# Kernel optimization log

Measured on AMD Instinct MI355X. Metric: run time of the kernel, lower is better.

## Reference

```python
import jax, jax.numpy as jnp
import numpy as np

# ---- physics constraint targets (constants, precomputed with numpy) ----
_ARC = np.array([[-1,-1,-1],[2,2,2],[-1,-1,-1]], np.float32)
_CURV5 = np.array([[0,0,-1,0,0],[0,-1,2,-1,0],[-1,2,4,2,-1],[0,-1,2,-1,0],[0,0,-1,0,0]], np.float32)
_RAD = np.array([[0,-1,0],[-1,4,-1],[0,-1,0]], np.float32)
_TAN = np.array([[-1,0,-1],[0,4,0],[-1,0,-1]], np.float32)

def _bilinear_1d(a, out_n):
    # torch F.interpolate bilinear, align_corners=False, along axis 0
    n = a.shape[0]
    src = (np.arange(out_n) + 0.5) * n / out_n - 0.5
    i0 = np.clip(np.floor(src).astype(int), 0, n - 1)
    i1 = np.clip(i0 + 1, 0, n - 1)
    f = np.clip(src - np.floor(src), 0.0, 1.0).astype(np.float32)
    shp = (out_n,) + (1,) * (a.ndim - 1)
    return a[i0] * (1 - f).reshape(shp) + a[i1] * f.reshape(shp)

_CURV3 = _bilinear_1d(_bilinear_1d(_CURV5, 3).T, 3).T  # 5x5 -> 3x3 separable bilinear
CONSTRAINTS = jnp.asarray(np.stack([_ARC, _CURV3, _RAD, _TAN]))  # [4,3,3]

NUM_HEADS = 4
PHYSICS_WEIGHT = 0.1


def setup_inputs() -> dict:
    key = jax.random.key(0)
    ks = jax.random.split(key, 6)
    B, N, C = 8, 1024, 256
    return {
        "x": jax.random.normal(ks[0], (B, N, C), jnp.float32),
        "qkv_w": jax.random.normal(ks[1], (3 * C, C), jnp.float32) * (C ** -0.5),
        "qkv_b": jax.random.normal(ks[2], (3 * C,), jnp.float32) * 0.02,
        "proj_w": jax.random.normal(ks[3], (C, C), jnp.float32) * (C ** -0.5),
        "proj_b": jax.random.normal(ks[4], (C,), jnp.float32) * 0.02,
        "kernels": jax.random.normal(ks[5], (4, 3, 3), jnp.float32) * 0.1,
        "H": 32,
        "W": 32,
    }


def _physics_prior(x, kernels, H, W):
    # Original: depthwise conv each channel with each kernel, mean over kernels,
    # mean over channels, sigmoid, outer product. Conv + means are linear, so
    # mean-over-kernels and mean-over-channels commute with the (shared-kernel)
    # depthwise conv: conv(mean_C(x), mean_k(kernels)).
    B, N, C = x.shape
    xm = x.mean(axis=2).reshape(B, 1, H, W)            # [B,1,H,W]
    kmean = kernels.mean(axis=0)[None, None]           # [1,1,3,3] (OIHW)
    conv = jax.lax.conv_general_dilated(
        xm, kmean, window_strides=(1, 1), padding=((1, 1), (1, 1)),
        dimension_numbers=("NCHW", "OIHW", "NCHW"))
    amap = jax.nn.sigmoid(conv.reshape(B, N))          # [B,N]
    return amap[:, :, None] * amap[:, None, :]         # [B,N,N]


def _reg_loss(kernels):
    mse = jnp.mean((kernels - CONSTRAINTS) ** 2, axis=(1, 2)).sum()
    l1 = 0.01 * jnp.abs(kernels).sum()
    return mse + l1


def reference(x, qkv_w, qkv_b, proj_w, proj_b, kernels, H, W):
    B, N, C = x.shape
    hd = C // NUM_HEADS
    scale = hd ** -0.5
    qkv = (x @ qkv_w.T + qkv_b).reshape(B, N, 3, NUM_HEADS, hd)
    qkv = qkv.transpose(2, 0, 3, 1, 4)                 # [3,B,h,N,hd]
    q, k, v = qkv[0], qkv[1], qkv[2]
    attn = jnp.einsum("bhnd,bhmd->bhnm", q, k) * scale  # [B,h,N,N]
    prior = _physics_prior(x, kernels, H, W)            # [B,N,N]
    attn = attn + PHYSICS_WEIGHT * prior[:, None]
    attn = jax.nn.softmax(attn, axis=-1)                # dropout: eval mode (identity)
    out = jnp.einsum("bhnm,bhmd->bhnd", attn, v)
    out = out.transpose(0, 2, 1, 3).reshape(B, N, C)
    out = out @ proj_w.T + proj_b
    attention_weights = attn.mean(axis=1)               # [B,N,N]
    return out, attention_weights, _reg_loss(kernels)
```

## Files before the change

kernel.cpp:

```cpp
#include <hip/hip_runtime.h>
#include <cstdint>

typedef _Float16 h16;
typedef __attribute__((ext_vector_type(8))) _Float16 f16x8;
typedef __attribute__((ext_vector_type(4))) _Float16 f16x4;
typedef __attribute__((ext_vector_type(4))) float f32x4;

__global__ void k_xm(const float* __restrict__ x, float* __restrict__ xm) {
  int row = (blockIdx.x << 2) + (threadIdx.x >> 6);
  int lane = threadIdx.x & 63;
  const float* p = x + (size_t)row * 256;
  float s = p[lane] + p[lane + 64] + p[lane + 128] + p[lane + 192];
#pragma unroll
  for (int off = 32; off; off >>= 1) s += __shfl_xor(s, off);
  if (lane == 0) xm[row] = s * (1.0f / 256.0f);
}

__global__ void k_amap(const float* __restrict__ xm,
                       const float* __restrict__ kern,
                       float* __restrict__ amap) {
  int idx = blockIdx.x * 256 + threadIdx.x;
  int b = idx >> 10, n = idx & 1023;
  int y = n >> 5, xq = n & 31;
  float km[9];
#pragma unroll
  for (int i = 0; i < 9; ++i)
    km[i] = 0.25f * (kern[i] + kern[9 + i] + kern[18 + i] + kern[27 + i]);
  float acc = 0.f;
#pragma unroll
  for (int dy = 0; dy < 3; ++dy) {
#pragma unroll
    for (int dx = 0; dx < 3; ++dx) {
      int yy = y + dy - 1, xx = xq + dx - 1;
      if (yy >= 0 && yy < 32 && xx >= 0 && xx < 32)
        acc += km[dy * 3 + dx] * xm[(b << 10) + (yy << 5) + xx];
    }
  }
  amap[idx] = 1.0f / (1.0f + __expf(-acc));
}

__global__ void k_cast(const float* __restrict__ x, const float* __restrict__ qw,
                       const float* __restrict__ pw, h16* __restrict__ xh,
                       h16* __restrict__ qwh, h16* __restrict__ pwh) {
  int i4 = blockIdx.x * 256 + threadIdx.x;
  const float* src;
  h16* dst;
  int off;
  if (i4 < 524288) { src = x; dst = xh; off = i4; }
  else if (i4 < 573440) { src = qw; dst = qwh; off = i4 - 524288; }
  else { src = pw; dst = pwh; off = i4 - 573440; }
  float4 v = ((const float4*)src)[off];
  f16x4 o = {(h16)v.x, (h16)v.y, (h16)v.z, (h16)v.w};
  ((f16x4*)dst)[off] = o;
}

__global__ __launch_bounds__(128) void k_qkv(
    const h16* __restrict__ xh, const h16* __restrict__ qwh,
    const float* __restrict__ bias, h16* __restrict__ Qh,
    h16* __restrict__ Kh, h16* __restrict__ Vt) {
  const int w = threadIdx.x >> 6, lane = threadIdx.x & 63;
  const int g = lane >> 4, li = lane & 15;
  const int tile = blockIdx.x * 2 + w;
  const int tr = tile & 255, tc = tile >> 8;
  const int r0 = tr * 32, c0 = tc * 64;
  f32x4 acc[2][4];
#pragma unroll
  for (int mr = 0; mr < 2; ++mr)
#pragma unroll
    for (int nc = 0; nc < 4; ++nc) acc[mr][nc] = {0.f, 0.f, 0.f, 0.f};
  for (int ks = 0; ks < 8; ++ks) {
    int k0 = ks * 32 + g * 8;
    f16x8 a[2], bf[4];
#pragma unroll
    for (int mr = 0; mr < 2; ++mr)
      a[mr] = *(const f16x8*)(xh + (size_t)(r0 + mr * 16 + li) * 256 + k0);
#pragma unroll
    for (int nc = 0; nc < 4; ++nc)
      bf[nc] = *(const f16x8*)(qwh + (size_t)(c0 + nc * 16 + li) * 256 + k0);
#pragma unroll
    for (int mr = 0; mr < 2; ++mr)
#pragma unroll
      for (int nc = 0; nc < 4; ++nc)
        acc[mr][nc] = __builtin_amdgcn_mfma_f32_16x16x32_f16(a[mr], bf[nc],
                                                             acc[mr][nc], 0, 0, 0);
  }
  const int which = c0 >> 8;
  const int hh = (c0 >> 6) & 3;
#pragma unroll
  for (int nc = 0; nc < 4; ++nc) {
    int d = nc * 16 + li;
    float bv = bias[c0 + d];
#pragma unroll
    for (int mr = 0; mr < 2; ++mr) {
#pragma unroll
      for (int r = 0; r < 4; ++r) {
        int m = r0 + mr * 16 + g * 4 + r;
        int bq = m >> 10, n = m & 1023;
        float v = acc[mr][nc][r] + bv;
        size_t base = ((size_t)(bq * 4 + hh)) << 16;
        if (which == 0) Qh[base + (size_t)n * 64 + d] = (h16)v;
        else if (which == 1) Kh[base + (size_t)n * 64 + d] = (h16)v;
        else Vt[base + (size_t)d * 1024 + n] = (h16)v;
      }
    }
  }
}

__device__ __forceinline__ void compute_S(const h16* __restrict__ Kp,
                                          const float* __restrict__ am, int j0,
                                          const f16x8 (&qf)[2][2],
                                          const float (&am_r)[2][4], int g,
                                          int li, f32x4 (&s)[2][4]) {
  f16x8 kf[4][2];
#pragma unroll
  for (int nc = 0; nc < 4; ++nc)
#pragma unroll
    for (int ks = 0; ks < 2; ++ks)
      kf[nc][ks] =
          *(const f16x8*)(Kp + (size_t)(j0 + nc * 16 + li) * 64 + ks * 32 + g * 8);
#pragma unroll
  for (int mr = 0; mr < 2; ++mr)
#pragma unroll
    for (int nc = 0; nc < 4; ++nc) {
      f32x4 a = {0.f, 0.f, 0.f, 0.f};
      a = __builtin_amdgcn_mfma_f32_16x16x32_f16(qf[mr][0], kf[nc][0], a, 0, 0, 0);
      a = __builtin_amdgcn_mfma_f32_16x16x32_f16(qf[mr][1], kf[nc][1], a, 0, 0, 0);
      s[mr][nc] = a;
    }
#pragma unroll
  for (int mr = 0; mr < 2; ++mr)
#pragma unroll
    for (int nc = 0; nc < 4; ++nc) {
      float amc = am[j0 + nc * 16 + li];
#pragma unroll
      for (int r = 0; r < 4; ++r)
        s[mr][nc][r] = s[mr][nc][r] * 0.125f + am_r[mr][r] * amc;
    }
}

__global__ __launch_bounds__(256) void k_attn(
    const h16* __restrict__ Qh, const h16* __restrict__ Kh,
    const h16* __restrict__ Vt, const float* __restrict__ amap,
    h16* __restrict__ OHh, float* __restrict__ AW) {
  __shared__ __align__(16) unsigned char Pst[4][4096];
  const int tid = threadIdx.x;
  const int h = tid >> 6, lane = tid & 63, g = lane >> 4, li = lane & 15;
  const int b = blockIdx.x & 7, rt = blockIdx.x >> 3;
  const int r0 = rt * 32;
  const size_t base = ((size_t)(b * 4 + h)) << 16;
  const h16* Kp = Kh + base;
  const float* am = amap + (b << 10);

  f16x8 qf[2][2];
#pragma unroll
  for (int mr = 0; mr < 2; ++mr)
#pragma unroll
    for (int ks = 0; ks < 2; ++ks)
      qf[mr][ks] =
          *(const f16x8*)(Qh + base + (size_t)(r0 + mr * 16 + li) * 64 + ks * 32 + g * 8);

  float am_r[2][4];
#pragma unroll
  for (int mr = 0; mr < 2; ++mr)
#pragma unroll
    for (int r = 0; r < 4; ++r)
      am_r[mr][r] = 0.1f * am[r0 + mr * 16 + g * 4 + r];

  float m_run[2][4], l_run[2][4];
#pragma unroll
  for (int mr = 0; mr < 2; ++mr)
#pragma unroll
    for (int r = 0; r < 4; ++r) { m_run[mr][r] = -1e30f; l_run[mr][r] = 0.f; }

  for (int jt = 0; jt < 16; ++jt) {
    f32x4 s[2][4];
    compute_S(Kp, am, jt * 64, qf, am_r, g, li, s);
#pragma unroll
    for (int mr = 0; mr < 2; ++mr) {
#pragma unroll
      for (int r = 0; r < 4; ++r) {
        float mx = fmaxf(fmaxf(s[mr][0][r], s[mr][1][r]),
                         fmaxf(s[mr][2][r], s[mr][3][r]));
        mx = fmaxf(mx, __shfl_xor(mx, 1));
        mx = fmaxf(mx, __shfl_xor(mx, 2));
        mx = fmaxf(mx, __shfl_xor(mx, 4));
        mx = fmaxf(mx, __shfl_xor(mx, 8));
        float mnew = fmaxf(m_run[mr][r], mx);
        float ps = __expf(s[mr][0][r] - mnew) + __expf(s[mr][1][r] - mnew) +
                   __expf(s[mr][2][r] - mnew) + __expf(s[mr][3][r] - mnew);
        ps += __shfl_xor(ps, 1);
        ps += __shfl_xor(ps, 2);
        ps += __shfl_xor(ps, 4);
        ps += __shfl_xor(ps, 8);
        l_run[mr][r] = l_run[mr][r] * __expf(m_run[mr][r] - mnew) + ps;
        m_run[mr][r] = mnew;
      }
    }
  }
  float rinv[2][4];
#pragma unroll
  for (int mr = 0; mr < 2; ++mr)
#pragma unroll
    for (int r = 0; r < 4; ++r) rinv[mr][r] = 1.0f / l_run[mr][r];

  f32x4 o[2][4];
#pragma unroll
  for (int mr = 0; mr < 2; ++mr)
#pragma unroll
    for (int nd = 0; nd < 4; ++nd) o[mr][nd] = {0.f, 0.f, 0.f, 0.f};

  for (int jt = 0; jt < 16; ++jt) {
    const int j0 = jt * 64;
    f32x4 s[2][4];
    compute_S(Kp, am, j0, qf, am_r, g, li, s);
    __syncthreads();
#pragma unroll
    for (int mr = 0; mr < 2; ++mr) {
#pragma unroll
      for (int nc = 0; nc < 4; ++nc) {
        int colb = (nc * 16 + li) * 2;
#pragma unroll
        for (int r = 0; r < 4; ++r) {
          int row = mr * 16 + g * 4 + r;
          float p = __expf(s[mr][nc][r] - m_run[mr][r]) * rinv[mr][r];
          *(h16*)(&Pst[h][(row << 7) + (colb ^ ((row & 7) << 4))]) = (h16)p;
        }
      }
    }
    __syncthreads();
    f16x8 vf[4][2], af[2][2];
#pragma unroll
    for (int nd = 0; nd < 4; ++nd)
#pragma unroll
      for (int ks = 0; ks < 2; ++ks)
        vf[nd][ks] = *(const f16x8*)(Vt + base + (size_t)(nd * 16 + li) * 1024 +
                                     j0 + ks * 32 + g * 8);
#pragma unroll
    for (int mr = 0; mr < 2; ++mr)
#pragma unroll
      for (int ks = 0; ks < 2; ++ks) {
        int row = mr * 16 + li;
        int colb = (ks * 32 + g * 8) * 2;
        af[mr][ks] =
            *(const f16x8*)(&Pst[h][(row << 7) + (colb ^ ((row & 7) << 4))]);
      }
#pragma unroll
    for (int mr = 0; mr < 2; ++mr)
#pragma unroll
      for (int nd = 0; nd < 4; ++nd) {
        o[mr][nd] = __builtin_amdgcn_mfma_f32_16x16x32_f16(af[mr][0], vf[nd][0],
                                                           o[mr][nd], 0, 0, 0);
        o[mr][nd] = __builtin_amdgcn_mfma_f32_16x16x32_f16(af[mr][1], vf[nd][1],
                                                           o[mr][nd], 0, 0, 0);
      }
    {
      int row = tid >> 3, c8 = (tid & 7) * 8;
      float sum[8] = {0.f, 0.f, 0.f, 0.f, 0.f, 0.f, 0.f, 0.f};
#pragma unroll
      for (int hh = 0; hh < 4; ++hh) {
        f16x8 q = *(const f16x8*)(&Pst[hh][(row << 7) +
                                           ((c8 * 2) ^ ((row & 7) << 4))]);
#pragma unroll
        for (int i = 0; i < 8; ++i) sum[i] += (float)q[i];
      }
      float* dst = AW + ((size_t)b << 20) + (size_t)(r0 + row) * 1024 + j0 + c8;
      float4 o1 = {0.25f * sum[0], 0.25f * sum[1], 0.25f * sum[2], 0.25f * sum[3]};
      float4 o2 = {0.25f * sum[4], 0.25f * sum[5], 0.25f * sum[6], 0.25f * sum[7]};
      *(float4*)dst = o1;
      *(float4*)(dst + 4) = o2;
    }
  }
#pragma unroll
  for (int mr = 0; mr < 2; ++mr)
#pragma unroll
    for (int nd = 0; nd < 4; ++nd)
#pragma unroll
      for (int r = 0; r < 4; ++r)
        OHh[(size_t)((b << 10) + r0 + mr * 16 + g * 4 + r) * 256 + h * 64 +
            nd * 16 + li] = (h16)o[mr][nd][r];
}

__global__ __launch_bounds__(128) void k_proj(const h16* __restrict__ OHh,
                                              const h16* __restrict__ pwh,
                                              const float* __restrict__ bias,
                                              float* __restrict__ out) {
  const int w = threadIdx.x >> 6, lane = threadIdx.x & 63;
  const int g = lane >> 4, li = lane & 15;
  const int tile = blockIdx.x * 2 + w;
  const int tc = tile & 3, tr = tile >> 2;
  const int r0 = tr * 32, c0 = tc * 64;
  f32x4 acc[2][4];
#pragma unroll
  for (int mr = 0; mr < 2; ++mr)
#pragma unroll
    for (int nc = 0; nc < 4; ++nc) acc[mr][nc] = {0.f, 0.f, 0.f, 0.f};
  for (int ks = 0; ks < 8; ++ks) {
    int k0 = ks * 32 + g * 8;
    f16x8 a[2], bf[4];
#pragma unroll
    for (int mr = 0; mr < 2; ++mr)
      a[mr] = *(const f16x8*)(OHh + (size_t)(r0 + mr * 16 + li) * 256 + k0);
#pragma unroll
    for (int nc = 0; nc < 4; ++nc)
      bf[nc] = *(const f16x8*)(pwh + (size_t)(c0 + nc * 16 + li) * 256 + k0);
#pragma unroll
    for (int mr = 0; mr < 2; ++mr)
#pragma unroll
      for (int nc = 0; nc < 4; ++nc)
        acc[mr][nc] = __builtin_amdgcn_mfma_f32_16x16x32_f16(a[mr], bf[nc],
                                                             acc[mr][nc], 0, 0, 0);
  }
#pragma unroll
  for (int nc = 0; nc < 4; ++nc) {
    int c = c0 + nc * 16 + li;
    float bv = bias[c];
#pragma unroll
    for (int mr = 0; mr < 2; ++mr)
#pragma unroll
      for (int r = 0; r < 4; ++r) {
        int m = r0 + mr * 16 + g * 4 + r;
        out[(size_t)m * 256 + c] = acc[mr][nc][r] + bv;
      }
  }
}

__global__ void k_reg(const float* __restrict__ kern, float* __restrict__ out) {
  const float Cst[36] = {
      -1.f, -1.f, -1.f, 2.f, 2.f, 2.f, -1.f, -1.f, -1.f,
      -0.11111111f, 0.f, -0.11111111f, 0.f, 4.f, 0.f,
      -0.11111111f, 0.f, -0.11111111f,
      0.f, -1.f, 0.f, -1.f, 4.f, -1.f, 0.f, -1.f, 0.f,
      -1.f, 0.f, -1.f, 0.f, 4.f, 0.f, -1.f, 0.f, -1.f};
  int t = threadIdx.x;
  float v = 0.f;
  if (t < 36) {
    float kv = kern[t];
    float d = kv - Cst[t];
    v = d * d * (1.0f / 9.0f) + 0.01f * fabsf(kv);
  }
#pragma unroll
  for (int off = 32; off; off >>= 1) v += __shfl_xor(v, off);
  if (t == 0) out[0] = v;
}

extern "C" void kernel_launch(void* const* d_in, const int* in_sizes, int n_in,
                              void* d_out, int out_size, void* d_ws,
                              size_t ws_size, hipStream_t stream) {
  const float* x = (const float*)d_in[0];
  const float* qkv_w = (const float*)d_in[1];
  const float* qkv_b = (const float*)d_in[2];
  const float* proj_w = (const float*)d_in[3];
  const float* proj_b = (const float*)d_in[4];
  const float* kern = (const float*)d_in[5];

  float* out = (float*)d_out;
  float* aw = out + 2097152;
  float* rl = out + 10485760;

  float* xm = (float*)d_ws;
  float* amap = xm + 8192;
  h16* xh = (h16*)(amap + 8192);
  h16* qwh = xh + 2097152;
  h16* pwh = qwh + 196608;
  h16* Qh = pwh + 65536;
  h16* Kh = Qh + 2097152;
  h16* Vt = Kh + 2097152;
  h16* OHh = Vt + 2097152;

  k_xm<<<2048, 256, 0, stream>>>(x, xm);
  k_amap<<<32, 256, 0, stream>>>(xm, kern, amap);
  k_cast<<<2304, 256, 0, stream>>>(x, qkv_w, proj_w, xh, qwh, pwh);
  k_qkv<<<1536, 128, 0, stream>>>(xh, qwh, qkv_b, Qh, Kh, Vt);
  k_attn<<<256, 256, 0, stream>>>(Qh, Kh, Vt, amap, OHh, aw);
  k_proj<<<512, 128, 0, stream>>>(OHh, pwh, proj_b, out);
  k_reg<<<1, 64, 0, stream>>>(kern, rl);
}
```

Baseline: 215.2 us.

## Single-pass attention using Cauchy-Schwarz max bound and deferred normalization

Replaces the two-pass online-softmax attention with a single pass. A precomputed upper bound on each row's logits (query norm times the per-head max key norm, plus the prior term) serves as a fixed softmax shift, so no running max is needed. Unnormalized probabilities go to a global fp16 buffer, and a separate kernel applies the row normalization and averages over heads to write the attention weights. The key range is also split across two waves per head with an LDS reduction, and the x->fp16 cast is fused with the channel mean. The cost is extra global traffic for P and a risk that the loose bound underflows exp2 for rows whose logits sit far below it.

```diff
diff --git a/kernel.cpp b/kernel.cpp
--- a/kernel.cpp
+++ b/kernel.cpp
@@ -6,14 +6,35 @@
 typedef __attribute__((ext_vector_type(4))) _Float16 f16x4;
 typedef __attribute__((ext_vector_type(4))) float f32x4;
 
-__global__ void k_xm(const float* __restrict__ x, float* __restrict__ xm) {
-  int row = (blockIdx.x << 2) + (threadIdx.x >> 6);
-  int lane = threadIdx.x & 63;
-  const float* p = x + (size_t)row * 256;
-  float s = p[lane] + p[lane + 64] + p[lane + 128] + p[lane + 192];
-#pragma unroll
-  for (int off = 32; off; off >>= 1) s += __shfl_xor(s, off);
-  if (lane == 0) xm[row] = s * (1.0f / 256.0f);
+#define L2E 1.44269504f
+
+__global__ void k_cast(const float* __restrict__ x, const float* __restrict__ qw,
+                       const float* __restrict__ pw, h16* __restrict__ xh,
+                       h16* __restrict__ qwh, h16* __restrict__ pwh,
+                       float* __restrict__ xm) {
+  int bid = blockIdx.x, tid = threadIdx.x;
+  if (bid < 2048) {
+    int i4 = bid * 256 + tid;
+    float4 v = ((const float4*)x)[i4];
+    f16x4 o = {(h16)v.x, (h16)v.y, (h16)v.z, (h16)v.w};
+    ((f16x4*)xh)[i4] = o;
+    float s = v.x + v.y + v.z + v.w;
+#pragma unroll
+    for (int off = 32; off; off >>= 1) s += __shfl_xor(s, off);
+    if ((tid & 63) == 0) xm[i4 >> 6] = s * (1.0f / 256.0f);
+  } else {
+    int i4 = (bid - 2048) * 256 + tid;
+    if (i4 < 49152) {
+      float4 v = ((const float4*)qw)[i4];
+      f16x4 o = {(h16)v.x, (h16)v.y, (h16)v.z, (h16)v.w};
+      ((f16x4*)qwh)[i4] = o;
+    } else {
+      int j = i4 - 49152;
+      float4 v = ((const float4*)pw)[j];
+      f16x4 o = {(h16)v.x, (h16)v.y, (h16)v.z, (h16)v.w};
+      ((f16x4*)pwh)[j] = o;
+    }
+  }
 }
 
 __global__ void k_amap(const float* __restrict__ xm,
@@ -37,21 +58,6 @@
     }
   }
   amap[idx] = 1.0f / (1.0f + __expf(-acc));
-}
-
-__global__ void k_cast(const float* __restrict__ x, const float* __restrict__ qw,
-                       const float* __restrict__ pw, h16* __restrict__ xh,
-                       h16* __restrict__ qwh, h16* __restrict__ pwh) {
-  int i4 = blockIdx.x * 256 + threadIdx.x;
-  const float* src;
-  h16* dst;
-  int off;
-  if (i4 < 524288) { src = x; dst = xh; off = i4; }
-  else if (i4 < 573440) { src = qw; dst = qwh; off = i4 - 524288; }
-  else { src = pw; dst = pwh; off = i4 - 573440; }
-  float4 v = ((const float4*)src)[off];
-  f16x4 o = {(h16)v.x, (h16)v.y, (h16)v.z, (h16)v.w};
-  ((f16x4*)dst)[off] = o;
 }
 
 __global__ __launch_bounds__(128) void k_qkv(
@@ -106,178 +112,197 @@
   }
 }
 
-__device__ __forceinline__ void compute_S(const h16* __restrict__ Kp,
-                                          const float* __restrict__ am, int j0,
-                                          const f16x8 (&qf)[2][2],
-                                          const float (&am_r)[2][4], int g,
-                                          int li, f32x4 (&s)[2][4]) {
-  f16x8 kf[4][2];
-#pragma unroll
-  for (int nc = 0; nc < 4; ++nc)
-#pragma unroll
-    for (int ks = 0; ks < 2; ++ks)
-      kf[nc][ks] =
-          *(const f16x8*)(Kp + (size_t)(j0 + nc * 16 + li) * 64 + ks * 32 + g * 8);
-#pragma unroll
-  for (int mr = 0; mr < 2; ++mr)
+__global__ void k_knorm(const h16* __restrict__ Kh, float* __restrict__ Kmaxb) {
+  __shared__ float red[4];
+  const int tid = threadIdx.x;
+  const h16* base = Kh + ((size_t)blockIdx.x << 16);
+  float mx = 0.f;
+#pragma unroll
+  for (int i = 0; i < 4; ++i) {
+    int n = i * 256 + tid;
+    float s2 = 0.f;
+#pragma unroll
+    for (int ks = 0; ks < 8; ++ks) {
+      f16x8 v = *(const f16x8*)(base + (size_t)n * 64 + ks * 8);
+#pragma unroll
+      for (int e = 0; e < 8; ++e) {
+        float f = (float)v[e];
+        s2 += f * f;
+      }
+    }
+    mx = fmaxf(mx, s2);
+  }
+#pragma unroll
+  for (int off = 32; off; off >>= 1) mx = fmaxf(mx, __shfl_xor(mx, off));
+  if ((tid & 63) == 0) red[tid >> 6] = mx;
+  __syncthreads();
+  if (tid == 0) {
+    mx = fmaxf(fmaxf(red[0], red[1]), fmaxf(red[2], red[3]));
+    Kmaxb[blockIdx.x] = sqrtf(mx);
+  }
+}
+
+__global__ __launch_bounds__(512, 4) void k_attn(
+    const h16* __restrict__ Qh, const h16* __restrict__ Kh,
+    const h16* __restrict__ Vt, const float* __restrict__ amap,
+    const float* __restrict__ Kmaxb, h16* __restrict__ Pg,
+    float* __restrict__ rinvb, h16* __restrict__ OHh) {
+  __shared__ float am_s[1024];
+  __shared__ float Lsh[4][2][16];
+  __shared__ float Osh[4][16][64];
+  __shared__ __align__(16) unsigned char Pst[8][2048];
+
+  const int tid = threadIdx.x;
+  const int wave = tid >> 6, lane = tid & 63, g = lane >> 4, li = lane & 15;
+  const int h = wave >> 1, jh = wave & 1;
+  const int b = blockIdx.x & 7, rt = blockIdx.x >> 3;
+  const int r0 = rt * 16;
+  const int bh = b * 4 + h;
+  const size_t base = ((size_t)bh) << 16;
+
+  am_s[tid] = amap[(b << 10) + tid];
+  am_s[tid + 512] = amap[(b << 10) + 512 + tid];
+  __syncthreads();
+
+  f16x8 qf[2];
+#pragma unroll
+  for (int ks = 0; ks < 2; ++ks)
+    qf[ks] = *(const f16x8*)(Qh + base + (size_t)(r0 + li) * 64 + ks * 32 + g * 8);
+
+  float nq2 = 0.f;
+#pragma unroll
+  for (int ks = 0; ks < 2; ++ks)
+#pragma unroll
+    for (int e = 0; e < 8; ++e) {
+      float f = (float)qf[ks][e];
+      nq2 += f * f;
+    }
+  nq2 += __shfl_xor(nq2, 16);
+  nq2 += __shfl_xor(nq2, 32);
+  float c_li = 0.125f * sqrtf(nq2) * Kmaxb[bh] + 0.11f;
+  float cr2[4], amr2[4];
+#pragma unroll
+  for (int r = 0; r < 4; ++r) {
+    cr2[r] = __shfl(c_li, g * 4 + r) * L2E;
+    amr2[r] = 0.1f * L2E * am_s[r0 + g * 4 + r];
+  }
+
+  float lpart[4] = {0.f, 0.f, 0.f, 0.f};
+  f32x4 o[4];
+#pragma unroll
+  for (int nd = 0; nd < 4; ++nd) o[nd] = {0.f, 0.f, 0.f, 0.f};
+
+  for (int jj = 0; jj < 8; ++jj) {
+    const int j0 = (jh * 8 + jj) << 6;
+    f16x8 kf[4][2];
+#pragma unroll
+    for (int nc = 0; nc < 4; ++nc)
+#pragma unroll
+      for (int ks = 0; ks < 2; ++ks)
+        kf[nc][ks] = *(const f16x8*)(Kh + base + (size_t)(j0 + nc * 16 + li) * 64 +
+                                     ks * 32 + g * 8);
+    f32x4 s[4];
 #pragma unroll
     for (int nc = 0; nc < 4; ++nc) {
       f32x4 a = {0.f, 0.f, 0.f, 0.f};
-      a = __builtin_amdgcn_mfma_f32_16x16x32_f16(qf[mr][0], kf[nc][0], a, 0, 0, 0);
-      a = __builtin_amdgcn_mfma_f32_16x16x32_f16(qf[mr][1], kf[nc][1], a, 0, 0, 0);
-      s[mr][nc] = a;
-    }
-#pragma unroll
-  for (int mr = 0; mr < 2; ++mr)
+      a = __builtin_amdgcn_mfma_f32_16x16x32_f16(qf[0], kf[nc][0], a, 0, 0, 0);
+      a = __builtin_amdgcn_mfma_f32_16x16x32_f16(qf[1], kf[nc][1], a, 0, 0, 0);
+      s[nc] = a;
+    }
 #pragma unroll
     for (int nc = 0; nc < 4; ++nc) {
-      float amc = am[j0 + nc * 16 + li];
+      float amc = am_s[j0 + nc * 16 + li];
+      int colb = (nc * 16 + li) * 2;
+#pragma unroll
+      for (int r = 0; r < 4; ++r) {
+        float p = exp2f(s[nc][r] * (0.125f * L2E) + amr2[r] * amc - cr2[r]);
+        lpart[r] += p;
+        int row = g * 4 + r;
+        *(h16*)(&Pst[wave][(row << 7) + (colb ^ ((row & 7) << 4))]) = (h16)p;
+      }
+    }
+    f16x8 af[2];
+#pragma unroll
+    for (int ks = 0; ks < 2; ++ks) {
+      int cb = (ks * 32 + g * 8) * 2;
+      af[ks] = *(const f16x8*)(&Pst[wave][(li << 7) + (cb ^ ((li & 7) << 4))]);
+      *(f16x8*)(Pg + ((size_t)bh << 20) + (size_t)(r0 + li) * 1024 + j0 +
+                ks * 32 + g * 8) = af[ks];
+    }
+#pragma unroll
+    for (int nd = 0; nd < 4; ++nd) {
+      f16x8 v0 = *(const f16x8*)(Vt + base + (size_t)(nd * 16 + li) * 1024 + j0 +
+                                 g * 8);
+      f16x8 v1 = *(const f16x8*)(Vt + base + (size_t)(nd * 16 + li) * 1024 + j0 +
+                                 32 + g * 8);
+      o[nd] = __builtin_amdgcn_mfma_f32_16x16x32_f16(af[0], v0, o[nd], 0, 0, 0);
+      o[nd] = __builtin_amdgcn_mfma_f32_16x16x32_f16(af[1], v1, o[nd], 0, 0, 0);
+    }
+  }
+
+#pragma unroll
+  for (int r = 0; r < 4; ++r) {
+    lpart[r] += __shfl_xor(lpart[r], 1);
+    lpart[r] += __shfl_xor(lpart[r], 2);
+    lpart[r] += __shfl_xor(lpart[r], 4);
+    lpart[r] += __shfl_xor(lpart[r], 8);
+  }
+  if (li == 0) {
+#pragma unroll
+    for (int r = 0; r < 4; ++r) Lsh[h][jh][g * 4 + r] = lpart[r];
+  }
+  __syncthreads();
+  float rinv[4];
+#pragma unroll
+  for (int r = 0; r < 4; ++r)
+    rinv[r] = 1.0f / (Lsh[h][0][g * 4 + r] + Lsh[h][1][g * 4 + r]);
+  if (jh == 1) {
+#pragma unroll
+    for (int nd = 0; nd < 4; ++nd)
+#pragma unroll
+      for (int r = 0; r < 4; ++r) Osh[h][g * 4 + r][nd * 16 + li] = o[nd][r];
+  }
+  __syncthreads();
+  if (jh == 0) {
+#pragma unroll
+    for (int nd = 0; nd < 4; ++nd)
+#pragma unroll
+      for (int r = 0; r < 4; ++r) {
+        float v = (o[nd][r] + Osh[h][g * 4 + r][nd * 16 + li]) * rinv[r];
+        OHh[(size_t)((b << 10) + r0 + g * 4 + r) * 256 + h * 64 + nd * 16 + li] =
+            (h16)v;
+      }
+    if (li == 0) {
 #pragma unroll
       for (int r = 0; r < 4; ++r)
-        s[mr][nc][r] = s[mr][nc][r] * 0.125f + am_r[mr][r] * amc;
-    }
-}
-
-__global__ __launch_bounds__(256) void k_attn(
-    const h16* __restrict__ Qh, const h16* __restrict__ Kh,
-    const h16* __restrict__ Vt, const float* __restrict__ amap,
-    h16* __restrict__ OHh, float* __restrict__ AW) {
-  __shared__ __align__(16) unsigned char Pst[4][4096];
-  const int tid = threadIdx.x;
-  const int h = tid >> 6, lane = tid & 63, g = lane >> 4, li = lane & 15;
-  const int b = blockIdx.x & 7, rt = blockIdx.x >> 3;
-  const int r0 = rt * 32;
-  const size_t base = ((size_t)(b * 4 + h)) << 16;
-  const h16* Kp = Kh + base;
-  const float* am = amap + (b << 10);
-
-  f16x8 qf[2][2];
-#pragma unroll
-  for (int mr = 0; mr < 2; ++mr)
-#pragma unroll
-    for (int ks = 0; ks < 2; ++ks)
-      qf[mr][ks] =
-          *(const f16x8*)(Qh + base + (size_t)(r0 + mr * 16 + li) * 64 + ks * 32 + g * 8);
-
-  float am_r[2][4];
-#pragma unroll
-  for (int mr = 0; mr < 2; ++mr)
-#pragma unroll
-    for (int r = 0; r < 4; ++r)
-      am_r[mr][r] = 0.1f * am[r0 + mr * 16 + g * 4 + r];
-
-  float m_run[2][4], l_run[2][4];
-#pragma unroll
-  for (int mr = 0; mr < 2; ++mr)
-#pragma unroll
-    for (int r = 0; r < 4; ++r) { m_run[mr][r] = -1e30f; l_run[mr][r] = 0.f; }
-
-  for (int jt = 0; jt < 16; ++jt) {
-    f32x4 s[2][4];
-    compute_S(Kp, am, jt * 64, qf, am_r, g, li, s);
-#pragma unroll
-    for (int mr = 0; mr < 2; ++mr) {
-#pragma unroll
-      for (int r = 0; r < 4; ++r) {
-        float mx = fmaxf(fmaxf(s[mr][0][r], s[mr][1][r]),
-                         fmaxf(s[mr][2][r], s[mr][3][r]));
-        mx = fmaxf(mx, __shfl_xor(mx, 1));
-        mx = fmaxf(mx, __shfl_xor(mx, 2));
-        mx = fmaxf(mx, __shfl_xor(mx, 4));
-        mx = fmaxf(mx, __shfl_xor(mx, 8));
-        float mnew = fmaxf(m_run[mr][r], mx);
-        float ps = __expf(s[mr][0][r] - mnew) + __expf(s[mr][1][r] - mnew) +
-                   __expf(s[mr][2][r] - mnew) + __expf(s[mr][3][r] - mnew);
-        ps += __shfl_xor(ps, 1);
-        ps += __shfl_xor(ps, 2);
-        ps += __shfl_xor(ps, 4);
-        ps += __shfl_xor(ps, 8);
-        l_run[mr][r] = l_run[mr][r] * __expf(m_run[mr][r] - mnew) + ps;
-        m_run[mr][r] = mnew;
-      }
-    }
-  }
-  float rinv[2][4];
-#pragma unroll
-  for (int mr = 0; mr < 2; ++mr)
-#pragma unroll
-    for (int r = 0; r < 4; ++r) rinv[mr][r] = 1.0f / l_run[mr][r];
-
-  f32x4 o[2][4];
-#pragma unroll
-  for (int mr = 0; mr < 2; ++mr)
-#pragma unroll
-    for (int nd = 0; nd < 4; ++nd) o[mr][nd] = {0.f, 0.f, 0.f, 0.f};
-
-  for (int jt = 0; jt < 16; ++jt) {
-    const int j0 = jt * 64;
-    f32x4 s[2][4];
-    compute_S(Kp, am, j0, qf, am_r, g, li, s);
-    __syncthreads();
-#pragma unroll
-    for (int mr = 0; mr < 2; ++mr) {
-#pragma unroll
-      for (int nc = 0; nc < 4; ++nc) {
-        int colb = (nc * 16 + li) * 2;
-#pragma unroll
-        for (int r = 0; r < 4; ++r) {
-          int row = mr * 16 + g * 4 + r;
-          float p = __expf(s[mr][nc][r] - m_run[mr][r]) * rinv[mr][r];
-          *(h16*)(&Pst[h][(row << 7) + (colb ^ ((row & 7) << 4))]) = (h16)p;
-        }
-      }
-    }
-    __syncthreads();
-    f16x8 vf[4][2], af[2][2];
-#pragma unroll
-    for (int nd = 0; nd < 4; ++nd)
-#pragma unroll
-      for (int ks = 0; ks < 2; ++ks)
-        vf[nd][ks] = *(const f16x8*)(Vt + base + (size_t)(nd * 16 + li) * 1024 +
-                                     j0 + ks * 32 + g * 8);
-#pragma unroll
-    for (int mr = 0; mr < 2; ++mr)
-#pragma unroll
-      for (int ks = 0; ks < 2; ++ks) {
-        int row = mr * 16 + li;
-        int colb = (ks * 32 + g * 8) * 2;
-        af[mr][ks] =
-            *(const f16x8*)(&Pst[h][(row << 7) + (colb ^ ((row & 7) << 4))]);
-      }
-#pragma unroll
-    for (int mr = 0; mr < 2; ++mr)
-#pragma unroll
-      for (int nd = 0; nd < 4; ++nd) {
-        o[mr][nd] = __builtin_amdgcn_mfma_f32_16x16x32_f16(af[mr][0], vf[nd][0],
-                                                           o[mr][nd], 0, 0, 0);
-        o[mr][nd] = __builtin_amdgcn_mfma_f32_16x16x32_f16(af[mr][1], vf[nd][1],
-                                                           o[mr][nd], 0, 0, 0);
-      }
-    {
-      int row = tid >> 3, c8 = (tid & 7) * 8;
-      float sum[8] = {0.f, 0.f, 0.f, 0.f, 0.f, 0.f, 0.f, 0.f};
-#pragma unroll
-      for (int hh = 0; hh < 4; ++hh) {
-        f16x8 q = *(const f16x8*)(&Pst[hh][(row << 7) +
-                                           ((c8 * 2) ^ ((row & 7) << 4))]);
-#pragma unroll
-        for (int i = 0; i < 8; ++i) sum[i] += (float)q[i];
-      }
-      float* dst = AW + ((size_t)b << 20) + (size_t)(r0 + row) * 1024 + j0 + c8;
-      float4 o1 = {0.25f * sum[0], 0.25f * sum[1], 0.25f * sum[2], 0.25f * sum[3]};
-      float4 o2 = {0.25f * sum[4], 0.25f * sum[5], 0.25f * sum[6], 0.25f * sum[7]};
-      *(float4*)dst = o1;
-      *(float4*)(dst + 4) = o2;
-    }
-  }
-#pragma unroll
-  for (int mr = 0; mr < 2; ++mr)
-#pragma unroll
-    for (int nd = 0; nd < 4; ++nd)
-#pragma unroll
-      for (int r = 0; r < 4; ++r)
-        OHh[(size_t)((b << 10) + r0 + mr * 16 + g * 4 + r) * 256 + h * 64 +
-            nd * 16 + li] = (h16)o[mr][nd][r];
+        rinvb[((size_t)bh << 10) + r0 + g * 4 + r] = rinv[r];
+    }
+  }
+}
+
+__global__ void k_awnorm(const h16* __restrict__ Pg,
+                         const float* __restrict__ rinvb,
+                         float* __restrict__ AW) {
+  int idx = blockIdx.x * 256 + threadIdx.x;
+  int b = idx >> 17;
+  int rem = idx & 131071;
+  int i = rem >> 7;
+  int jc = (rem & 127) << 3;
+  size_t rowbase = ((size_t)i << 10) + jc;
+  float sum[8] = {0.f, 0.f, 0.f, 0.f, 0.f, 0.f, 0.f, 0.f};
+#pragma unroll
+  for (int h = 0; h < 4; ++h) {
+    int bh = b * 4 + h;
+    f16x8 pu = *(const f16x8*)(Pg + (((size_t)bh) << 20) + rowbase);
+    float rv = 0.25f * rinvb[((size_t)bh << 10) + i];
+#pragma unroll
+    for (int e = 0; e < 8; ++e) sum[e] += (float)pu[e] * rv;
+  }
+  float* dst = AW + (((size_t)b) << 20) + rowbase;
+  float4 o1 = {sum[0], sum[1], sum[2], sum[3]};
+  float4 o2 = {sum[4], sum[5], sum[6], sum[7]};
+  *(float4*)dst = o1;
+  *(float4*)(dst + 4) = o2;
 }
 
 __global__ __launch_bounds__(128) void k_proj(const h16* __restrict__ OHh,
@@ -359,19 +384,23 @@
 
   float* xm = (float*)d_ws;
   float* amap = xm + 8192;
-  h16* xh = (h16*)(amap + 8192);
+  float* rinvb = amap + 8192;
+  float* Kmaxb = rinvb + 32768;
+  h16* xh = (h16*)(Kmaxb + 64);
   h16* qwh = xh + 2097152;
   h16* pwh = qwh + 196608;
   h16* Qh = pwh + 65536;
   h16* Kh = Qh + 2097152;
   h16* Vt = Kh + 2097152;
   h16* OHh = Vt + 2097152;
-
-  k_xm<<<2048, 256, 0, stream>>>(x, xm);
+  h16* Pg = OHh + 2097152;
+
+  k_cast<<<2304, 256, 0, stream>>>(x, qkv_w, proj_w, xh, qwh, pwh, xm);
   k_amap<<<32, 256, 0, stream>>>(xm, kern, amap);
-  k_cast<<<2304, 256, 0, stream>>>(x, qkv_w, proj_w, xh, qwh, pwh);
   k_qkv<<<1536, 128, 0, stream>>>(xh, qwh, qkv_b, Qh, Kh, Vt);
-  k_attn<<<256, 256, 0, stream>>>(Qh, Kh, Vt, amap, OHh, aw);
+  k_knorm<<<32, 256, 0, stream>>>(Kh, Kmaxb);
+  k_attn<<<512, 512, 0, stream>>>(Qh, Kh, Vt, amap, Kmaxb, Pg, rinvb, OHh);
+  k_awnorm<<<4096, 256, 0, stream>>>(Pg, rinvb, aw);
   k_proj<<<512, 128, 0, stream>>>(OHh, pwh, proj_b, out);
   k_reg<<<1, 64, 0, stream>>>(kern, rl);
 }
```

After: 222.2 us. 3.3% more time.
